# Kernel optimization log

Measured on AMD Instinct MI355X. Metric: run time of the kernel, lower is better.

## Reference

```python
import jax, jax.numpy as jnp
import numpy as np

N, E, B, ROWS, IN, HID, JKO, FEAT, OH, OUT = 200000, 6400000, 64, 128, 128, 6, 4, 2560, 20, 2

def _leaky(x, s):
    return jnp.where(x >= 0, x, s * x)

def _ln(x, g, b, eps=1e-5):
    mu = jnp.mean(x, -1, keepdims=True)
    v = jnp.mean((x - mu) ** 2, -1, keepdims=True)
    return (x - mu) * jax.lax.rsqrt(v + eps) * g + b

def setup_inputs():
    key = jax.random.key(0)
    ks = jax.random.split(key, 32)
    def w(k, shape, fan_in):
        return jax.random.normal(k, shape, jnp.float32) * (1.0 / np.sqrt(fan_in))
    inp = {
        'x': jax.random.normal(ks[0], (N, IN), jnp.float32),
        'edge_index': jax.random.randint(ks[1], (2, E), 0, N, jnp.int32),
        'batch': jnp.sort(jax.random.randint(ks[2], (N,), 0, B, jnp.int32)),
        'features': jax.random.normal(ks[3], (B, ROWS, FEAT), jnp.float32),
        'one_hot': jax.random.uniform(ks[4], (B, OH), jnp.float32),
        # GATv2Conv params (heads=1)
        'W_l': w(ks[5], (IN, HID), IN), 'b_l': jnp.zeros((HID,)),
        'W_r': w(ks[6], (IN, HID), IN), 'b_r': jnp.zeros((HID,)),
        'att': w(ks[7], (HID,), HID), 'conv_b': jnp.zeros((HID,)),
        # BasicGNN final lin after JK (6 -> 4)
        'jk_W': w(ks[8], (HID, JKO), HID), 'jk_b': jnp.zeros((JKO,)),
        # MLP chain on features
        'l1_W': w(ks[9], (FEAT, 256), FEAT), 'l1_b': jnp.zeros((256,)),
        'ln1_g': jnp.ones((256,)), 'ln1_b': jnp.zeros((256,)),
        'l2_W': w(ks[10], (256, 64), 256), 'l2_b': jnp.zeros((64,)),
        'ln2_g': jnp.ones((64,)), 'ln2_b': jnp.zeros((64,)),
        'l3_W': w(ks[11], (64, 8), 64), 'l3_b': jnp.zeros((8,)),
        'ln3_g': jnp.ones((8,)), 'ln3_b': jnp.zeros((8,)),
        # flattening: rows*8 -> 32
        'fl_W': w(ks[12], (ROWS * 8, 32), ROWS * 8), 'fl_b': jnp.zeros((32,)),
        'ln4_g': jnp.ones((32,)), 'ln4_b': jnp.zeros((32,)),
        # output: 4 + 32 + 20 = 56 -> OUT
        'out_W': w(ks[13], (56, OUT), 56), 'out_b': jnp.zeros((OUT,)),
    }
    return inp

def _forward(x, features, one_hot, W_l, b_l, W_r, b_r, att, conv_b, jk_W, jk_b,
             l1_W, l1_b, ln1_g, ln1_b, l2_W, l2_b, ln2_g, ln2_b, l3_W, l3_b, ln3_g, ln3_b,
             fl_W, fl_b, ln4_g, ln4_b, out_W, out_b, edge_index, batch):
    n = x.shape[0]
    # GATv2Conv, heads=1: separate source/target transforms
    xl = x @ W_l + b_l  # [N,6] source/message features
    xr = x @ W_r + b_r  # [N,6] target features
    loops = jnp.arange(n, dtype=edge_index.dtype)
    src = jnp.concatenate([edge_index[0], loops])  # add self loops
    dst = jnp.concatenate([edge_index[1], loops])
    e = _leaky(xl[src] + xr[dst], 0.2)             # [E+N,6]
    score = e @ att                                 # [E+N]
    m = jax.lax.stop_gradient(jax.ops.segment_max(score, dst, num_segments=n))
    p = jnp.exp(score - m[dst])
    z = jax.ops.segment_sum(p, dst, num_segments=n)
    alpha = p / z[dst]                              # segment softmax over incoming edges
    agg = jax.ops.segment_sum(alpha[:, None] * xl[src], dst, num_segments=n) + conv_b
    x1 = _leaky(agg, 0.01)                          # BasicGNN act ('leakyrelu')
    # JK-LSTM with a single layer collapses to identity (softmax over 1 element)
    h = x1 @ jk_W + jk_b                            # [N,4]
    # global mean pool per graph
    nb = features.shape[0]
    sums = jax.ops.segment_sum(h, batch, num_segments=nb)
    cnt = jax.ops.segment_sum(jnp.ones((n,), h.dtype), batch, num_segments=nb)
    xgcn = sums / jnp.maximum(cnt, 1.0)[:, None]    # [B,4]
    # MLP on features (dropout = identity in eval)
    f = _leaky(_ln(features @ l1_W + l1_b, ln1_g, ln1_b), 0.01)
    f = _leaky(_ln(f @ l2_W + l2_b, ln2_g, ln2_b), 0.01)
    f = _leaky(_ln(f @ l3_W + l3_b, ln3_g, ln3_b), 0.01)  # [B,ROWS,8]
    flat = f.reshape(nb, -1)
    xf = _leaky(_ln(flat @ fl_W + fl_b, ln4_g, ln4_b), 0.01)  # [B,32]
    cat = jnp.concatenate([xgcn, xf, one_hot], axis=1)        # [B,56]
    return cat @ out_W + out_b

def reference(x, features, one_hot, W_l, b_l, W_r, b_r, att, conv_b, jk_W, jk_b,
              l1_W, l1_b, ln1_g, ln1_b, l2_W, l2_b, ln2_g, ln2_b, l3_W, l3_b, ln3_g, ln3_b,
              fl_W, fl_b, ln4_g, ln4_b, out_W, out_b, edge_index, batch):
    return _forward(x, features, one_hot, W_l, b_l, W_r, b_r, att, conv_b, jk_W, jk_b,
                    l1_W, l1_b, ln1_g, ln1_b, l2_W, l2_b, ln2_g, ln2_b, l3_W, l3_b, ln3_g, ln3_b,
                    fl_W, fl_b, ln4_g, ln4_b, out_W, out_b, edge_index, batch)
```

## Files before the change

kernel.cpp:

```cpp
#include <hip/hip_runtime.h>
#include <cstdint>
#include <cstddef>

#define N_NODES 200000
#define N_EDGES 6400000
#define NB      64
#define MROWS   8192
#define FEAT    2560

#define BSZ   256
#define NBK   782
#define EBLK  512
#define ETILE 12500
#define BCAP  8960
#define NXB   768
#define GEMMB 256
#define MLPB  64

typedef __attribute__((ext_vector_type(8))) short bf16x8;
typedef __attribute__((ext_vector_type(4))) float f32x4;

__device__ __forceinline__ unsigned short bf16rne(float f) {
    unsigned u = __builtin_bit_cast(unsigned, f);
    u += 0x7fffu + ((u >> 16) & 1u);
    return (unsigned short)(u >> 16);
}

__device__ __forceinline__ float bf16f(unsigned short h) {
    return __builtin_bit_cast(float, (unsigned)h << 16);
}

__device__ __forceinline__ void async_cp16(const void* g, void* l) {
    __builtin_amdgcn_global_load_lds(
        (const __attribute__((address_space(1))) unsigned int*)g,
        (__attribute__((address_space(3))) unsigned int*)l, 16, 0, 0);
}

__device__ __forceinline__ void edge_acc(
    uint4 g, const float* xrd, const float* attv, float& z, float* agg)
{
    float xls[6];
    xls[0] = __builtin_bit_cast(float, g.x << 16);
    xls[1] = __builtin_bit_cast(float, g.x & 0xffff0000u);
    xls[2] = __builtin_bit_cast(float, g.y << 16);
    xls[3] = __builtin_bit_cast(float, g.y & 0xffff0000u);
    xls[4] = __builtin_bit_cast(float, g.z << 16);
    xls[5] = __builtin_bit_cast(float, g.z & 0xffff0000u);
    float sc = 0.f;
#pragma unroll
    for (int j = 0; j < 6; j++) {
        float e = xls[j] + xrd[j];
        e = (e >= 0.f) ? e : 0.2f * e;
        sc += attv[j] * e;
    }
    const float p = __expf(sc);
    z += p;
#pragma unroll
    for (int j = 0; j < 6; j++) agg[j] += p * xls[j];
}


__device__ __forceinline__ void nx_body(
    const int nxi, const int nstride,
    const float* __restrict__ x,
    const float* __restrict__ Wl, const float* __restrict__ bl,
    const float* __restrict__ Wr, const float* __restrict__ br,
    unsigned short* __restrict__ xlb, float* __restrict__ xr)
{
    const int t = threadIdx.x;
    const int l = t & 15;

    float wl[48], wr[48];
#pragma unroll
    for (int q = 0; q < 12; q++) {
        *(float4*)&wl[q * 4] = *(const float4*)(Wl + 48 * l + 4 * q);
        *(float4*)&wr[q * 4] = *(const float4*)(Wr + 48 * l + 4 * q);
    }
    for (int g = nxi; g < N_NODES / 16; g += nstride) {
        const int node = g * 16 + (t >> 4);
        float xv[8];
        *(float4*)&xv[0] = *(const float4*)(x + (size_t)node * 128 + l * 8);
        *(float4*)&xv[4] = *(const float4*)(x + (size_t)node * 128 + l * 8 + 4);

        float al[6] = {}, ar[6] = {};
#pragma unroll
        for (int i = 0; i < 8; i++) {
#pragma unroll
            for (int j = 0; j < 6; j++) {
                al[j] += xv[i] * wl[i * 6 + j];
                ar[j] += xv[i] * wr[i * 6 + j];
            }
        }
#pragma unroll
        for (int off = 8; off >= 1; off >>= 1) {
#pragma unroll
            for (int j = 0; j < 6; j++) {
                al[j] += __shfl_xor(al[j], off);
                ar[j] += __shfl_xor(ar[j], off);
            }
        }
        if (l == 0) {
            union { unsigned short h[8]; uint4 v; } u;
#pragma unroll
            for (int j = 0; j < 6; j++) u.h[j] = bf16rne(al[j] + bl[j]);
            u.h[6] = 0; u.h[7] = 0;
            *(uint4*)(xlb + (size_t)node * 8) = u.v;
            float4 r0; float2 r1;
            r0.x = ar[0] + br[0]; r0.y = ar[1] + br[1];
            r0.z = ar[2] + br[2]; r0.w = ar[3] + br[3];
            r1.x = ar[4] + br[4]; r1.y = ar[5] + br[5];
            *(float4*)(xr + (size_t)node * 8) = r0;
            *(float2*)(xr + (size_t)node * 8 + 4) = r1;
        }
    }
}

__device__ __forceinline__ void eb_body(
    const int bid, char* smem,
    const int* __restrict__ ei, int* __restrict__ cursor, int* __restrict__ pairs)
{
    int* sorted = (int*)smem;
    int* hb     = sorted + ETILE;
    int* cur    = hb + NBK + 1;
    int* gbl    = cur + NBK;
    int* wsum   = gbl + NBK;
    const int t = threadIdx.x;
    const int lane = t & 63, wid = t >> 6;
    const int base = bid * ETILE;

    for (int b = t; b < NBK; b += 256) cur[b] = 0;
    __syncthreads();

    for (int i = t; i < ETILE; i += 256)
        atomicAdd(&cur[ei[N_EDGES + base + i] >> 8], 1);
    __syncthreads();

    int c[4]; int lsum = 0;
#pragma unroll
    for (int q = 0; q < 4; q++) {
        const int b = 4 * t + q;
        c[q] = (b < NBK) ? cur[b] : 0;
        lsum += c[q];
    }
    int v = lsum;
#pragma unroll
    for (int d = 1; d < 64; d <<= 1) {
        const int o = __shfl_up(v, d);
        if (lane >= d) v += o;
    }
    if (lane == 63) wsum[wid] = v;
    __syncthreads();
    int off = 0;
#pragma unroll
    for (int w = 0; w < 3; w++) if (w < wid) off += wsum[w];
    int run = off + v - lsum;

    int mygb[4];
#pragma unroll
    for (int q = 0; q < 4; q++) {
        const int b = 4 * t + q;
        mygb[q] = (b < NBK && c[q] > 0) ? atomicAdd(&cursor[b], c[q]) : 0;
    }

#pragma unroll
    for (int q = 0; q < 4; q++) {
        const int b = 4 * t + q;
        if (b <= NBK) hb[b] = run;
        if (b < NBK) cur[b] = run;
        run += c[q];
    }
    __syncthreads();

    for (int i = t; i < ETILE; i += 256) {
        const int d = ei[N_EDGES + base + i];
        const int s = ei[base + i];
        const int pos = atomicAdd(&cur[d >> 8], 1);
        sorted[pos] = (s << 8) | (d & 255);
    }
#pragma unroll
    for (int q = 0; q < 4; q++) {
        const int b = 4 * t + q;
        if (b < NBK) gbl[b] = mygb[q];
    }
    __syncthreads();

    const int grp = t >> 4, gl = t & 15;
    for (int b = grp; b < NBK; b += 16) {
        const int st = hb[b];
        const int cnt = hb[b + 1] - st;
        int* dst = pairs + b * BCAP + gbl[b];
        for (int i = gl; i < cnt; i += 16)
            dst[i] = sorted[st + i];
    }
}

__device__ __forceinline__ void gemm_l1_body(
    const int bx, const int by, char* smem,
    const float* __restrict__ A, const unsigned short* __restrict__ Bt,
    const float* __restrict__ bias, float* __restrict__ C)
{
    unsigned short (*As)[64 * 64] = (unsigned short(*)[64 * 64])smem;
    unsigned short (*Bs)[128 * 64] =
        (unsigned short(*)[128 * 64])(smem + 2 * 64 * 64 * sizeof(short));
    const int K = FEAT, N = 256;
    const int t = threadIdx.x;
    const int w = t >> 6, l = t & 63;
    const int l15 = l & 15, quad = l >> 4;
    const int wm = (w & 1) * 32, wn = (w >> 1) * 64;
    const int gm0 = bx * 64;
    const int gn0 = by * 128;
    const int r8 = l >> 3;
    const int c8 = (l & 7) ^ r8;
    const int ar = t >> 2;
    const int ac0 = (t & 3) * 2;

    f32x4 acc[2][4];
#pragma unroll
    for (int mt = 0; mt < 2; mt++)
#pragma unroll
        for (int nt = 0; nt < 4; nt++) acc[mt][nt] = (f32x4){0.f, 0.f, 0.f, 0.f};

    const int niter = K / 64;

#pragma unroll
    for (int c = 0; c < 4; c++) {
        const int j = w * 4 + c;
        async_cp16(Bt + (size_t)(gn0 + j * 8 + r8) * K + c8 * 8, &Bs[0][j * 512]);
    }
    {
        const float* src = A + (size_t)(gm0 + ar) * K + ac0 * 8;
        float4 v0 = *(const float4*)src;
        float4 v1 = *(const float4*)(src + 4);
        float4 v2 = *(const float4*)(src + 8);
        float4 v3 = *(const float4*)(src + 12);
        union { unsigned short h[8]; uint4 u; } p0, p1;
        p0.h[0] = bf16rne(v0.x); p0.h[1] = bf16rne(v0.y);
        p0.h[2] = bf16rne(v0.z); p0.h[3] = bf16rne(v0.w);
        p0.h[4] = bf16rne(v1.x); p0.h[5] = bf16rne(v1.y);
        p0.h[6] = bf16rne(v1.z); p0.h[7] = bf16rne(v1.w);
        p1.h[0] = bf16rne(v2.x); p1.h[1] = bf16rne(v2.y);
        p1.h[2] = bf16rne(v2.z); p1.h[3] = bf16rne(v2.w);
        p1.h[4] = bf16rne(v3.x); p1.h[5] = bf16rne(v3.y);
        p1.h[6] = bf16rne(v3.z); p1.h[7] = bf16rne(v3.w);
        *(uint4*)&As[0][ar * 64 + ((ac0 + 0) ^ (ar & 7)) * 8] = p0.u;
        *(uint4*)&As[0][ar * 64 + ((ac0 + 1) ^ (ar & 7)) * 8] = p1.u;
    }

    int p = 0;
    for (int i = 0; i < niter; i++) {
        __syncthreads();
        const bool nxt = (i + 1 < niter);
        float4 v0, v1, v2, v3;
        if (nxt) {
            const int k1 = (i + 1) * 64;
#pragma unroll
            for (int c = 0; c < 4; c++) {
                const int j = w * 4 + c;
                async_cp16(Bt + (size_t)(gn0 + j * 8 + r8) * K + k1 + c8 * 8,
                           &Bs[p ^ 1][j * 512]);
            }
            const float* src = A + (size_t)(gm0 + ar) * K + k1 + ac0 * 8;
            v0 = *(const float4*)src;
            v1 = *(const float4*)(src + 4);
            v2 = *(const float4*)(src + 8);
            v3 = *(const float4*)(src + 12);
        }
#pragma unroll
        for (int kki = 0; kki < 2; kki++) {
            bf16x8 af[2], bfr[4];
#pragma unroll
            for (int mt = 0; mt < 2; mt++) {
                const int m = wm + mt * 16 + l15;
                af[mt] = *(const bf16x8*)&As[p][m * 64 + (((quad + 4 * kki) ^ (m & 7)) * 8)];
            }
#pragma unroll
            for (int nt = 0; nt < 4; nt++) {
                const int n = wn + nt * 16 + l15;
                bfr[nt] = *(const bf16x8*)&Bs[p][n * 64 + (((quad + 4 * kki) ^ (n & 7)) * 8)];
            }
#pragma unroll
            for (int mt = 0; mt < 2; mt++)
#pragma unroll
                for (int nt = 0; nt < 4; nt++)
                    acc[mt][nt] = __builtin_amdgcn_mfma_f32_16x16x32_bf16(
                        af[mt], bfr[nt], acc[mt][nt], 0, 0, 0);
        }
        if (nxt) {
            union { unsigned short h[8]; uint4 u; } p0, p1;
            p0.h[0] = bf16rne(v0.x); p0.h[1] = bf16rne(v0.y);
            p0.h[2] = bf16rne(v0.z); p0.h[3] = bf16rne(v0.w);
            p0.h[4] = bf16rne(v1.x); p0.h[5] = bf16rne(v1.y);
            p0.h[6] = bf16rne(v1.z); p0.h[7] = bf16rne(v1.w);
            p1.h[0] = bf16rne(v2.x); p1.h[1] = bf16rne(v2.y);
            p1.h[2] = bf16rne(v2.z); p1.h[3] = bf16rne(v2.w);
            p1.h[4] = bf16rne(v3.x); p1.h[5] = bf16rne(v3.y);
            p1.h[6] = bf16rne(v3.z); p1.h[7] = bf16rne(v3.w);
            *(uint4*)&As[p ^ 1][ar * 64 + ((ac0 + 0) ^ (ar & 7)) * 8] = p0.u;
            *(uint4*)&As[p ^ 1][ar * 64 + ((ac0 + 1) ^ (ar & 7)) * 8] = p1.u;
        }
        p ^= 1;
    }
#pragma unroll
    for (int nt = 0; nt < 4; nt++) {
        const int col = gn0 + wn + nt * 16 + l15;
        const float bv = bias[col];
#pragma unroll
        for (int mt = 0; mt < 2; mt++)
#pragma unroll
            for (int rr = 0; rr < 4; rr++) {
                const int row = gm0 + wm + mt * 16 + quad * 4 + rr;
                C[(size_t)row * N + col] = acc[mt][nt][rr] + bv;
            }
    }
}

__device__ __forceinline__ void br_body(
    const int bid, char* smem,
    const int* __restrict__ pairs, const int* __restrict__ cursor,
    const unsigned short* __restrict__ xlb, const float* __restrict__ xr,
    const float* __restrict__ att, const float* __restrict__ conv_b,
    const float* __restrict__ jkW, const float* __restrict__ jkb,
    const int* __restrict__ batch,
    float* __restrict__ gsum, float* __restrict__ gcnt)
{
    int* sorted = (int*)smem;
    int* hist   = sorted + BCAP;
    int* wtot   = hist + 256;
    const int t = threadIdx.x;
    const int lane = t & 63, wid = t >> 6;
    const int d0 = bid * BSZ + t;

    float xrd[6];
    if (d0 < N_NODES) {
        float4 a = *(const float4*)(xr + (size_t)d0 * 8);
        float2 b = *(const float2*)(xr + (size_t)d0 * 8 + 4);
        xrd[0] = a.x; xrd[1] = a.y; xrd[2] = a.z;
        xrd[3] = a.w; xrd[4] = b.x; xrd[5] = b.y;
    } else {
#pragma unroll
        for (int j = 0; j < 6; j++) xrd[j] = 0.f;
    }
    float attv[6];
#pragma unroll
    for (int j = 0; j < 6; j++) attv[j] = att[j];

    float z = 0.f, agg[6] = {};
    const uint4* xl4 = (const uint4*)xlb;
    const int e0 = bid * BCAP;
    const int e1 = e0 + cursor[bid];

    for (int c0 = e0; c0 < e1; c0 += BCAP) {
        const int rem = e1 - c0;
        const int cnt_chunk = (rem < BCAP) ? rem : BCAP;
        hist[t] = 0;
        __syncthreads();
        for (int i = t; i < cnt_chunk; i += 256)
            atomicAdd(&hist[pairs[c0 + i] & 255], 1);
        __syncthreads();
        const int h = hist[t];
        int v = h;
#pragma unroll
        for (int d = 1; d < 64; d <<= 1) {
            int o = __shfl_up(v, d);
            if (lane >= d) v += o;
        }
        if (lane == 63) wtot[wid] = v;
        __syncthreads();
        int off = 0;
#pragma unroll
        for (int wv = 0; wv < 3; wv++) if (wv < wid) off += wtot[wv];
        const int my_start = v - h + off;
        const int my_cnt = h;
        __syncthreads();
        hist[t] = my_start;
        __syncthreads();
        for (int i = t; i < cnt_chunk; i += 256) {
            const int pv = pairs[c0 + i];
            const int pos = atomicAdd(&hist[pv & 255], 1);
            sorted[pos] = ((unsigned)pv) >> 8;
        }
        __syncthreads();
        int i = 0;
        for (; i + 4 <= my_cnt; i += 4) {
            const int s0 = sorted[my_start + i];
            const int s1 = sorted[my_start + i + 1];
            const int s2 = sorted[my_start + i + 2];
            const int s3 = sorted[my_start + i + 3];
            const uint4 g0 = xl4[s0], g1 = xl4[s1], g2 = xl4[s2], g3 = xl4[s3];
            edge_acc(g0, xrd, attv, z, agg);
            edge_acc(g1, xrd, attv, z, agg);
            edge_acc(g2, xrd, attv, z, agg);
            edge_acc(g3, xrd, attv, z, agg);
        }
        for (; i < my_cnt; i++) {
            const uint4 g = xl4[sorted[my_start + i]];
            edge_acc(g, xrd, attv, z, agg);
        }
        __syncthreads();
    }

    float hh[4] = {0.f, 0.f, 0.f, 0.f};
    float cw = 0.f;
    int b = 0;
    if (d0 < N_NODES) {
        const uint4 g = xl4[d0];
        float xld[6];
        xld[0] = __builtin_bit_cast(float, g.x << 16);
        xld[1] = __builtin_bit_cast(float, g.x & 0xffff0000u);
        xld[2] = __builtin_bit_cast(float, g.y << 16);
        xld[3] = __builtin_bit_cast(float, g.y & 0xffff0000u);
        xld[4] = __builtin_bit_cast(float, g.z << 16);
        xld[5] = __builtin_bit_cast(float, g.z & 0xffff0000u);
        float sc = 0.f;
#pragma unroll
        for (int j = 0; j < 6; j++) {
            float e = xld[j] + xrd[j];
            e = (e >= 0.f) ? e : 0.2f * e;
            sc += attv[j] * e;
        }
        const float p = __expf(sc);
        const float zz = z + p;
#pragma unroll
        for (int c = 0; c < 4; c++) hh[c] = jkb[c];
#pragma unroll
        for (int j = 0; j < 6; j++) {
            float aj = (agg[j] + p * xld[j]) / zz + conv_b[j];
            aj = (aj >= 0.f) ? aj : 0.01f * aj;
#pragma unroll
            for (int c = 0; c < 4; c++) hh[c] += aj * jkW[j * 4 + c];
        }
        b = batch[d0];
        cw = 1.f;
    }
    const int b0 = __shfl(b, 0);
    if (__all(b == b0)) {
#pragma unroll
        for (int off2 = 32; off2 >= 1; off2 >>= 1) {
#pragma unroll
            for (int c = 0; c < 4; c++) hh[c] += __shfl_xor(hh[c], off2);
            cw += __shfl_xor(cw, off2);
        }
        if (lane == 0 && cw > 0.f) {
#pragma unroll
            for (int c = 0; c < 4; c++) atomicAdd(gsum + b0 * 4 + c, hh[c]);
            atomicAdd(gcnt + b0, cw);
        }
    } else if (cw > 0.f) {
#pragma unroll
        for (int c = 0; c < 4; c++) atomicAdd(gsum + b * 4 + c, hh[c]);
        atomicAdd(gcnt + b, cw);
    }
}

__device__ __forceinline__ void mlp_body(
    const int g, char* smem,
    const float* __restrict__ f1, const unsigned short* __restrict__ w2t,
    const float* __restrict__ ln1_g, const float* __restrict__ ln1_b,
    const float* __restrict__ l2_b,
    const float* __restrict__ ln2_g, const float* __restrict__ ln2_b,
    const float* __restrict__ l3_W, const float* __restrict__ l3_b,
    const float* __restrict__ ln3_g, const float* __restrict__ ln3_b,
    const float* __restrict__ fl_W, const float* __restrict__ fl_b,
    const float* __restrict__ ln4_g, const float* __restrict__ ln4_b,
    float* __restrict__ xf)
{
    unsigned short* W2 = (unsigned short*)smem;
    float* f3s = (float*)(smem + 32768);
    float* sp  = (float*)(smem + 32768 + 4096);
    const int t = threadIdx.x;
    const int w = t >> 6, l = t & 63;

    for (int i = t; i < 16384; i += 256) {
        const int j = i >> 8, k = i & 255;
        W2[k * 64 + j] = w2t[i];
    }
    const float4 g1 = *(const float4*)(ln1_g + 4 * l);
    const float4 b1 = *(const float4*)(ln1_b + 4 * l);
    const float bo2 = l2_b[l], g2 = ln2_g[l], b2 = ln2_b[l];
    float w3r[8];
    *(float4*)&w3r[0] = *(const float4*)(l3_W + l * 8);
    *(float4*)&w3r[4] = *(const float4*)(l3_W + l * 8 + 4);
    float g3[8], b3[8], bo3[8];
#pragma unroll
    for (int c = 0; c < 8; c++) {
        g3[c] = ln3_g[c]; b3[c] = ln3_b[c]; bo3[c] = l3_b[c];
    }
    __syncthreads();

    for (int r = w; r < 128; r += 4) {
        const size_t row = (size_t)g * 128 + r;
        const float4 v = *(const float4*)(f1 + row * 256 + 4 * l);
        float s = v.x + v.y + v.z + v.w;
        float s2 = v.x * v.x + v.y * v.y + v.z * v.z + v.w * v.w;
#pragma unroll
        for (int o = 32; o >= 1; o >>= 1) {
            s += __shfl_xor(s, o);
            s2 += __shfl_xor(s2, o);
        }
        const float mu = s * (1.0f / 256.0f);
        const float rs = rsqrtf(s2 * (1.0f / 256.0f) - mu * mu + 1e-5f);
        float y[4];
        y[0] = (v.x - mu) * rs * g1.x + b1.x;
        y[1] = (v.y - mu) * rs * g1.y + b1.y;
        y[2] = (v.z - mu) * rs * g1.z + b1.z;
        y[3] = (v.w - mu) * rs * g1.w + b1.w;
#pragma unroll
        for (int i = 0; i < 4; i++) y[i] = (y[i] >= 0.f) ? y[i] : 0.01f * y[i];

        float acc = bo2;
#pragma unroll 4
        for (int k0 = 0; k0 < 64; k0++) {
            const float yv0 = __shfl(y[0], k0);
            const float yv1 = __shfl(y[1], k0);
            const float yv2 = __shfl(y[2], k0);
            const float yv3 = __shfl(y[3], k0);
            const int kb = k0 * 256 + l;
            acc += yv0 * bf16f(W2[kb]);
            acc += yv1 * bf16f(W2[kb + 64]);
            acc += yv2 * bf16f(W2[kb + 128]);
            acc += yv3 * bf16f(W2[kb + 192]);
        }
        float s1 = acc, q1 = acc * acc;
#pragma unroll
        for (int o = 32; o >= 1; o >>= 1) {
            s1 += __shfl_xor(s1, o);
            q1 += __shfl_xor(q1, o);
        }
        const float mu2 = s1 * (1.0f / 64.0f);
        const float rs2 = rsqrtf(q1 * (1.0f / 64.0f) - mu2 * mu2 + 1e-5f);
        float y2 = (acc - mu2) * rs2 * g2 + b2;
        y2 = (y2 >= 0.f) ? y2 : 0.01f * y2;

        float p8[8];
#pragma unroll
        for (int c = 0; c < 8; c++) p8[c] = y2 * w3r[c];
#pragma unroll
        for (int o = 32; o >= 1; o >>= 1)
#pragma unroll
            for (int c = 0; c < 8; c++) p8[c] += __shfl_xor(p8[c], o);
#pragma unroll
        for (int c = 0; c < 8; c++) p8[c] += bo3[c];
        float s3 = 0.f;
#pragma unroll
        for (int c = 0; c < 8; c++) s3 += p8[c];
        const float mu3 = s3 * 0.125f;
        float q3 = 0.f;
#pragma unroll
        for (int c = 0; c < 8; c++) { const float d = p8[c] - mu3; q3 += d * d; }
        const float rs3 = rsqrtf(q3 * 0.125f + 1e-5f);
        if (l == 0) {
            float o8[8];
#pragma unroll
            for (int c = 0; c < 8; c++) {
                float yy = (p8[c] - mu3) * rs3 * g3[c] + b3[c];
                o8[c] = (yy >= 0.f) ? yy : 0.01f * yy;
            }
            *(float4*)&f3s[r * 8] = *(float4*)&o8[0];
            *(float4*)&f3s[r * 8 + 4] = *(float4*)&o8[4];
        }
    }
    __syncthreads();

    const int c = t & 31, part = t >> 5;
    float facc = 0.f;
    for (int k = part * 128; k < part * 128 + 128; k++)
        facc += f3s[k] * fl_W[k * 32 + c];
    sp[part * 32 + c] = facc;
    __syncthreads();
    if (t < 32) {
        float vv = fl_b[t];
#pragma unroll
        for (int p = 0; p < 8; p++) vv += sp[p * 32 + t];
        float ss = vv, ss2 = vv * vv;
#pragma unroll
        for (int o = 16; o >= 1; o >>= 1) {
            ss += __shfl_xor(ss, o);
            ss2 += __shfl_xor(ss2, o);
        }
        const float mu4 = ss * (1.0f / 32.0f);
        const float var4 = ss2 * (1.0f / 32.0f) - mu4 * mu4;
        float yy = (vv - mu4) * rsqrtf(var4 + 1e-5f) * ln4_g[t] + ln4_b[t];
        xf[g * 32 + t] = (yy >= 0.f) ? yy : 0.01f * yy;
    }
}


__global__ __launch_bounds__(256) void node_xform(
    const float* __restrict__ x,
    const float* __restrict__ Wl, const float* __restrict__ bl,
    const float* __restrict__ Wr, const float* __restrict__ br,
    unsigned short* __restrict__ xlb, float* __restrict__ xr)
{
    nx_body(blockIdx.x, N_NODES / 16, x, Wl, bl, Wr, br, xlb, xr);
}

__global__ __launch_bounds__(256) void edge_bucket(
    const int* __restrict__ ei, int* __restrict__ cursor, int* __restrict__ pairs)
{
    __shared__ __align__(16) char smem[59408];
    eb_body(blockIdx.x, smem, ei, cursor, pairs);
}

__global__ __launch_bounds__(256) void mfma_gemm_l1(
    const float* __restrict__ A, const unsigned short* __restrict__ Bt,
    const float* __restrict__ bias, float* __restrict__ C)
{
    __shared__ __align__(16) char smem[49152];
    gemm_l1_body(blockIdx.x, blockIdx.y, smem, A, Bt, bias, C);
}

__global__ __launch_bounds__(256) void bucket_reduce(
    const int* __restrict__ pairs, const int* __restrict__ cursor,
    const unsigned short* __restrict__ xlb, const float* __restrict__ xr,
    const float* __restrict__ att, const float* __restrict__ conv_b,
    const float* __restrict__ jkW, const float* __restrict__ jkb,
    const int* __restrict__ batch,
    float* __restrict__ gsum, float* __restrict__ gcnt)
{
    __shared__ __align__(16) char smem[36880];
    br_body(blockIdx.x, smem, pairs, cursor, xlb, xr, att, conv_b, jkW, jkb,
            batch, gsum, gcnt);
}

__global__ __launch_bounds__(256) void fused_front(
    const float* __restrict__ x,
    const float* __restrict__ Wl, const float* __restrict__ bl,
    const float* __restrict__ Wr, const float* __restrict__ br,
    unsigned short* __restrict__ xlb, float* __restrict__ xr,
    const int* __restrict__ ei, int* __restrict__ cursor, int* __restrict__ pairs,
    const float* __restrict__ A, const unsigned short* __restrict__ Bt,
    const float* __restrict__ bias, float* __restrict__ C)
{
    __shared__ __align__(16) char smem[59408];
    const int bid = blockIdx.x;
    const int role = bid % 3;
    const int q = bid / 3;
    if (role == 0) {
        eb_body(q, smem, ei, cursor, pairs);
    } else if (role == 1 && q < GEMMB) {
        gemm_l1_body(q & 127, q >> 7, smem, A, Bt, bias, C);
    } else {
        const int nxi = (role == 2) ? q : EBLK + (q - GEMMB);
        nx_body(nxi, NXB, x, Wl, bl, Wr, br, xlb, xr);
    }
}

__global__ __launch_bounds__(256, 4) void fused_back(
    const int* __restrict__ pairs, const int* __restrict__ cursor,
    const unsigned short* __restrict__ xlb, const float* __restrict__ xr,
    const float* __restrict__ att, const float* __restrict__ conv_b,
    const float* __restrict__ jkW, const float* __restrict__ jkb,
    const int* __restrict__ batch,
    float* __restrict__ gsum, float* __restrict__ gcnt,
    const float* __restrict__ f1, const unsigned short* __restrict__ w2t,
    const float* __restrict__ ln1_g, const float* __restrict__ ln1_b,
    const float* __restrict__ l2_b,
    const float* __restrict__ ln2_g, const float* __restrict__ ln2_b,
    const float* __restrict__ l3_W, const float* __restrict__ l3_b,
    const float* __restrict__ ln3_g, const float* __restrict__ ln3_b,
    const float* __restrict__ fl_W, const float* __restrict__ fl_b,
    const float* __restrict__ ln4_g, const float* __restrict__ ln4_b,
    float* __restrict__ xf)
{
    __shared__ __align__(16) char smem[37888];
    const int bid = blockIdx.x;
    const int q = bid / 13, r = bid % 13;
    if (r == 0 && q < MLPB) {
        mlp_body(q, smem, f1, w2t, ln1_g, ln1_b, l2_b, ln2_g, ln2_b,
                 l3_W, l3_b, ln3_g, ln3_b, fl_W, fl_b, ln4_g, ln4_b, xf);
    } else {
        const int brid = bid - ((q < MLPB) ? (q + (r > 0 ? 1 : 0)) : MLPB);
        br_body(brid, smem, pairs, cursor, xlb, xr, att, conv_b, jkW, jkb,
                batch, gsum, gcnt);
    }
}

__global__ __launch_bounds__(256) void castT(
    const float* __restrict__ W, unsigned short* __restrict__ Wt, int K, int N)
{
    const int k = blockIdx.x * 256 + threadIdx.x;
    const int n = blockIdx.y;
    if (k < K) Wt[(size_t)n * K + k] = bf16rne(W[(size_t)k * N + n]);
}


__global__ __launch_bounds__(256) void mfma_gemm_l2(
    const unsigned short* __restrict__ Ab, const unsigned short* __restrict__ Bt,
    const float* __restrict__ bias, float* __restrict__ C,
    int M, int N, int K)
{
    __shared__ unsigned short As[32 * 64];
    __shared__ unsigned short Bs[64 * 64];
    const int t = threadIdx.x;
    const int w = t >> 6, l = t & 63;
    const int l15 = l & 15, quad = l >> 4;
    const int gm0 = blockIdx.x * 32;
    const int gn0 = blockIdx.y * 64;
    const int r8 = l >> 3;
    const int c8 = (l & 7) ^ r8;

    f32x4 acc[2];
    acc[0] = (f32x4){0.f, 0.f, 0.f, 0.f};
    acc[1] = (f32x4){0.f, 0.f, 0.f, 0.f};

    for (int k0 = 0; k0 < K; k0 += 64) {
#pragma unroll
        for (int c = 0; c < 2; c++) {
            const int j = w * 2 + c;
            async_cp16(Bt + (size_t)(gn0 + j * 8 + r8) * K + k0 + c8 * 8,
                       &Bs[j * 512]);
        }
        async_cp16(Ab + (size_t)(gm0 + w * 8 + r8) * K + k0 + c8 * 8, &As[w * 512]);
        __syncthreads();
#pragma unroll
        for (int kki = 0; kki < 2; kki++) {
            bf16x8 af[2], bfr;
#pragma unroll
            for (int mt = 0; mt < 2; mt++) {
                const int m = mt * 16 + l15;
                af[mt] = *(const bf16x8*)&As[m * 64 + (((quad + 4 * kki) ^ (m & 7)) * 8)];
            }
            const int n = w * 16 + l15;
            bfr = *(const bf16x8*)&Bs[n * 64 + (((quad + 4 * kki) ^ (n & 7)) * 8)];
#pragma unroll
            for (int mt = 0; mt < 2; mt++)
                acc[mt] = __builtin_amdgcn_mfma_f32_16x16x32_bf16(
                    af[mt], bfr, acc[mt], 0, 0, 0);
        }
        __syncthreads();
    }
    const int col = gn0 + w * 16 + l15;
    const float bv = bias[col];
#pragma unroll
    for (int mt = 0; mt < 2; mt++)
#pragma unroll
        for (int rr = 0; rr < 4; rr++) {
            const int row = gm0 + mt * 16 + quad * 4 + rr;
            C[(size_t)row * N + col] = acc[mt][rr] + bv;
        }
}

__global__ __launch_bounds__(256) void ln_leaky_c256(
    const float* __restrict__ f, unsigned short* __restrict__ out,
    const float* __restrict__ g, const float* __restrict__ b)
{
    const int row = blockIdx.x;
    const int t = threadIdx.x;
    float v = f[(size_t)row * 256 + t];
    float s = v, s2 = v * v;
#pragma unroll
    for (int off = 32; off >= 1; off >>= 1) {
        s += __shfl_xor(s, off);
        s2 += __shfl_xor(s2, off);
    }
    __shared__ float ws[4], ws2[4];
    const int wid = t >> 6, lane = t & 63;
    if (lane == 0) { ws[wid] = s; ws2[wid] = s2; }
    __syncthreads();
    const float S = ws[0] + ws[1] + ws[2] + ws[3];
    const float S2 = ws2[0] + ws2[1] + ws2[2] + ws2[3];
    const float mu = S * (1.0f / 256.0f);
    const float var = S2 * (1.0f / 256.0f) - mu * mu;
    float y = (v - mu) * rsqrtf(var + 1e-5f) * g[t] + b[t];
    y = (y >= 0.f) ? y : 0.01f * y;
    out[(size_t)row * 256 + t] = bf16rne(y);
}

__global__ __launch_bounds__(256) void ln_leaky_c64(
    float* __restrict__ f, const float* __restrict__ g, const float* __restrict__ b)
{
    const int wid = threadIdx.x >> 6, lane = threadIdx.x & 63;
    const int row = blockIdx.x * 4 + wid;
    float v = f[(size_t)row * 64 + lane];
    float s = v, s2 = v * v;
#pragma unroll
    for (int off = 32; off >= 1; off >>= 1) {
        s += __shfl_xor(s, off);
        s2 += __shfl_xor(s2, off);
    }
    const float mu = s * (1.0f / 64.0f);
    const float var = s2 * (1.0f / 64.0f) - mu * mu;
    float y = (v - mu) * rsqrtf(var + 1e-5f) * g[lane] + b[lane];
    f[(size_t)row * 64 + lane] = (y >= 0.f) ? y : 0.01f * y;
}

__global__ __launch_bounds__(256) void l3_ln_leaky(
    const float* __restrict__ f2, const float* __restrict__ W3,
    const float* __restrict__ b3,
    const float* __restrict__ g, const float* __restrict__ b,
    float* __restrict__ f3)
{
    __shared__ float sW[64 * 8];
    const int t = threadIdx.x;
    sW[t] = W3[t]; sW[t + 256] = W3[t + 256];
    __syncthreads();
    const int row = blockIdx.x * 32 + (t >> 3);
    const int c = t & 7;
    float acc = b3[c];
    const float* fr = f2 + (size_t)row * 64;
#pragma unroll 8
    for (int k = 0; k < 64; k++) acc += fr[k] * sW[k * 8 + c];
    float s = acc, s2 = acc * acc;
#pragma unroll
    for (int off = 4; off >= 1; off >>= 1) {
        s += __shfl_xor(s, off);
        s2 += __shfl_xor(s2, off);
    }
    const float mu = s * (1.0f / 8.0f);
    const float var = s2 * (1.0f / 8.0f) - mu * mu;
    float y = (acc - mu) * rsqrtf(var + 1e-5f) * g[c] + b[c];
    f3[(size_t)row * 8 + c] = (y >= 0.f) ? y : 0.01f * y;
}

__global__ __launch_bounds__(256) void flat_ln_leaky(
    const float* __restrict__ f3, const float* __restrict__ W,
    const float* __restrict__ bb,
    const float* __restrict__ g, const float* __restrict__ b,
    float* __restrict__ xf)
{
    __shared__ float sf[1024];
    __shared__ float sp[8][32];
    const int t = threadIdx.x;
    const int gb = blockIdx.x;
    *(float4*)&sf[t * 4] = *(const float4*)(f3 + (size_t)gb * 1024 + t * 4);
    __syncthreads();
    const int c = t & 31, part = t >> 5;
    float acc = 0.f;
    for (int k = part * 128; k < part * 128 + 128; k++) acc += sf[k] * W[k * 32 + c];
    sp[part][c] = acc;
    __syncthreads();
    if (t < 32) {
        float v = bb[t];
#pragma unroll
        for (int p = 0; p < 8; p++) v += sp[p][t];
        float s = v, s2 = v * v;
#pragma unroll
        for (int off = 16; off >= 1; off >>= 1) {
            s += __shfl_xor(s, off);
            s2 += __shfl_xor(s2, off);
        }
        const float mu = s * (1.0f / 32.0f);
        const float var = s2 * (1.0f / 32.0f) - mu * mu;
        float y = (v - mu) * rsqrtf(var + 1e-5f) * g[t] + b[t];
        xf[gb * 32 + t] = (y >= 0.f) ? y : 0.01f * y;
    }
}

__global__ __launch_bounds__(128) void final_out(
    const float* __restrict__ gsum, const float* __restrict__ gcnt,
    const float* __restrict__ xf, const float* __restrict__ onehot,
    const float* __restrict__ Wo, const float* __restrict__ bo,
    float* __restrict__ out)
{
    const int t = threadIdx.x;
    const int gb = t >> 1, o = t & 1;
    float cnt = gcnt[gb];
    cnt = (cnt > 1.f) ? cnt : 1.f;
    float acc = bo[o];
#pragma unroll
    for (int j = 0; j < 4; j++)  acc += (gsum[gb * 4 + j] / cnt) * Wo[j * 2 + o];
#pragma unroll
    for (int j = 0; j < 32; j++) acc += xf[gb * 32 + j] * Wo[(4 + j) * 2 + o];
#pragma unroll
    for (int j = 0; j < 20; j++) acc += onehot[gb * 20 + j] * Wo[(36 + j) * 2 + o];
    out[t] = acc;
}

extern "C" void kernel_launch(void* const* d_in, const int* in_sizes, int n_in,
                              void* d_out, int out_size, void* d_ws, size_t ws_size,
                              hipStream_t stream)
{
    const float* x        = (const float*)d_in[0];
    const int*   ei       = (const int*)d_in[1];
    const int*   batch    = (const int*)d_in[2];
    const float* features = (const float*)d_in[3];
    const float* one_hot  = (const float*)d_in[4];
    const float* W_l   = (const float*)d_in[5];
    const float* b_l   = (const float*)d_in[6];
    const float* W_r   = (const float*)d_in[7];
    const float* b_r   = (const float*)d_in[8];
    const float* att   = (const float*)d_in[9];
    const float* conv_b = (const float*)d_in[10];
    const float* jk_W  = (const float*)d_in[11];
    const float* jk_b  = (const float*)d_in[12];
    const float* l1_W  = (const float*)d_in[13];
    const float* l1_b  = (const float*)d_in[14];
    const float* ln1_g = (const float*)d_in[15];
    const float* ln1_b = (const float*)d_in[16];
    const float* l2_W  = (const float*)d_in[17];
    const float* l2_b  = (const float*)d_in[18];
    const float* ln2_g = (const float*)d_in[19];
    const float* ln2_b = (const float*)d_in[20];
    const float* l3_W  = (const float*)d_in[21];
    const float* l3_b  = (const float*)d_in[22];
    const float* ln3_g = (const float*)d_in[23];
    const float* ln3_b = (const float*)d_in[24];
    const float* fl_W  = (const float*)d_in[25];
    const float* fl_b  = (const float*)d_in[26];
    const float* ln4_g = (const float*)d_in[27];
    const float* ln4_b = (const float*)d_in[28];
    const float* out_W = (const float*)d_in[29];
    const float* out_b = (const float*)d_in[30];
    (void)in_sizes; (void)n_in; (void)out_size;

    float* ws = (float*)d_ws;
    unsigned short* xlb = (unsigned short*)(ws + 0);
    float* xr   = ws + 800000;
    unsigned short* w1t = (unsigned short*)(ws + 2400000);
    unsigned short* w2t = (unsigned short*)(ws + 2727680);
    float* gsum   = ws + 2735872;
    float* gcnt   = ws + 2736128;
    int*   cursor = (int*)(ws + 2736192);
    int* pairs = (int*)(ws + 2737024);

    const bool fuse = ws_size >= (size_t)13481344 * 4;

    hipMemsetAsync(gsum, 0, 1102 * sizeof(float), stream);

    castT<<<dim3(10, 256), 256, 0, stream>>>(l1_W, w1t, FEAT, 256);
    castT<<<dim3(1, 64), 256, 0, stream>>>(l2_W, w2t, 256, 64);

    if (fuse) {
        float* f1 = ws + 9743744;
        float* xf = ws + 13479296;
        fused_front<<<EBLK + GEMMB + NXB, 256, 0, stream>>>(
            x, W_l, b_l, W_r, b_r, xlb, xr,
            ei, cursor, pairs,
            features, w1t, l1_b, f1);
        fused_back<<<NBK + MLPB, 256, 0, stream>>>(
            pairs, cursor, xlb, xr, att, conv_b, jk_W, jk_b, batch,
            gsum, gcnt,
            f1, w2t, ln1_g, ln1_b, l2_b, ln2_g, ln2_b,
            l3_W, l3_b, ln3_g, ln3_b, fl_W, fl_b, ln4_g, ln4_b, xf);
        final_out<<<1, 128, 0, stream>>>(gsum, gcnt, xf, one_hot, out_W, out_b,
                                         (float*)d_out);
    } else {
        float* f1           = ws + 2737024;
        unsigned short* f1b = (unsigned short*)(ws + 4834176);
        float* f2           = ws + 5358464;
        float* f3           = ws + 5882752;
        float* xf           = ws + 5948288;
        node_xform<<<N_NODES / 16, 256, 0, stream>>>(x, W_l, b_l, W_r, b_r,
                                                     xlb, xr);
        edge_bucket<<<EBLK, 256, 0, stream>>>(ei, cursor, pairs);
        bucket_reduce<<<NBK, 256, 0, stream>>>(pairs, cursor, xlb, xr, att,
                                               conv_b, jk_W, jk_b, batch,
                                               gsum, gcnt);
        mfma_gemm_l1<<<dim3(MROWS / 64, 2), 256, 0, stream>>>(
            features, w1t, l1_b, f1);
        ln_leaky_c256<<<MROWS, 256, 0, stream>>>(f1, f1b, ln1_g, ln1_b);
        mfma_gemm_l2<<<dim3(MROWS / 32, 1), 256, 0, stream>>>(
            f1b, w2t, l2_b, f2, MROWS, 64, 256);
        ln_leaky_c64<<<MROWS / 4, 256, 0, stream>>>(f2, ln2_g, ln2_b);
        l3_ln_leaky<<<MROWS / 32, 256, 0, stream>>>(f2, l3_W, l3_b,
                                                    ln3_g, ln3_b, f3);
        flat_ln_leaky<<<NB, 256, 0, stream>>>(f3, fl_W, fl_b, ln4_g, ln4_b, xf);
        final_out<<<1, 128, 0, stream>>>(gsum, gcnt, xf, one_hot, out_W, out_b,
                                         (float*)d_out);
    }
}
```

Baseline: 651.7 us.

## Split MLP tail into many row blocks and move flatten into final kernel

Measured after the change: 561.3 us. -13.9%, faster.

```diff
diff --git a/kernel.cpp b/kernel.cpp
--- a/kernel.cpp
+++ b/kernel.cpp
@@ -15,7 +15,7 @@
 #define BCAP  8960
 #define NXB   768
 #define GEMMB 256
-#define MLPB  64
+#define MLPRB 512
 
 typedef __attribute__((ext_vector_type(8))) short bf16x8;
 typedef __attribute__((ext_vector_type(4))) float f32x4;
@@ -452,27 +452,23 @@
     }
 }
 
-__device__ __forceinline__ void mlp_body(
-    const int g, char* smem,
+__device__ __forceinline__ void mlp_rows_body(
+    const int bid, char* smem,
     const float* __restrict__ f1, const unsigned short* __restrict__ w2t,
     const float* __restrict__ ln1_g, const float* __restrict__ ln1_b,
     const float* __restrict__ l2_b,
     const float* __restrict__ ln2_g, const float* __restrict__ ln2_b,
     const float* __restrict__ l3_W, const float* __restrict__ l3_b,
     const float* __restrict__ ln3_g, const float* __restrict__ ln3_b,
-    const float* __restrict__ fl_W, const float* __restrict__ fl_b,
-    const float* __restrict__ ln4_g, const float* __restrict__ ln4_b,
-    float* __restrict__ xf)
+    float* __restrict__ f3)
 {
     unsigned short* W2 = (unsigned short*)smem;
-    float* f3s = (float*)(smem + 32768);
-    float* sp  = (float*)(smem + 32768 + 4096);
     const int t = threadIdx.x;
     const int w = t >> 6, l = t & 63;
 
     for (int i = t; i < 16384; i += 256) {
         const int j = i >> 8, k = i & 255;
-        W2[k * 64 + j] = w2t[i];
+        W2[k * 66 + j] = w2t[i];
     }
     const float4 g1 = *(const float4*)(ln1_g + 4 * l);
     const float4 b1 = *(const float4*)(ln1_b + 4 * l);
@@ -487,9 +483,10 @@
     }
     __syncthreads();
 
-    for (int r = w; r < 128; r += 4) {
-        const size_t row = (size_t)g * 128 + r;
-        const float4 v = *(const float4*)(f1 + row * 256 + 4 * l);
+#pragma unroll 1
+    for (int i4 = 0; i4 < 4; i4++) {
+        const int row = bid * 16 + w * 4 + i4;
+        const float4 v = *(const float4*)(f1 + (size_t)row * 256 + 4 * l);
         float s = v.x + v.y + v.z + v.w;
         float s2 = v.x * v.x + v.y * v.y + v.z * v.z + v.w * v.w;
 #pragma unroll
@@ -514,11 +511,11 @@
             const float yv1 = __shfl(y[1], k0);
             const float yv2 = __shfl(y[2], k0);
             const float yv3 = __shfl(y[3], k0);
-            const int kb = k0 * 256 + l;
+            const int kb = k0 * 264 + l;
             acc += yv0 * bf16f(W2[kb]);
-            acc += yv1 * bf16f(W2[kb + 64]);
-            acc += yv2 * bf16f(W2[kb + 128]);
-            acc += yv3 * bf16f(W2[kb + 192]);
+            acc += yv1 * bf16f(W2[kb + 66]);
+            acc += yv2 * bf16f(W2[kb + 132]);
+            acc += yv3 * bf16f(W2[kb + 198]);
         }
         float s1 = acc, q1 = acc * acc;
 #pragma unroll
@@ -555,32 +552,9 @@
                 float yy = (p8[c] - mu3) * rs3 * g3[c] + b3[c];
                 o8[c] = (yy >= 0.f) ? yy : 0.01f * yy;
             }
-            *(float4*)&f3s[r * 8] = *(float4*)&o8[0];
-            *(float4*)&f3s[r * 8 + 4] = *(float4*)&o8[4];
-        }
-    }
-    __syncthreads();
-
-    const int c = t & 31, part = t >> 5;
-    float facc = 0.f;
-    for (int k = part * 128; k < part * 128 + 128; k++)
-        facc += f3s[k] * fl_W[k * 32 + c];
-    sp[part * 32 + c] = facc;
-    __syncthreads();
-    if (t < 32) {
-        float vv = fl_b[t];
-#pragma unroll
-        for (int p = 0; p < 8; p++) vv += sp[p * 32 + t];
-        float ss = vv, ss2 = vv * vv;
-#pragma unroll
-        for (int o = 16; o >= 1; o >>= 1) {
-            ss += __shfl_xor(ss, o);
-            ss2 += __shfl_xor(ss2, o);
-        }
-        const float mu4 = ss * (1.0f / 32.0f);
-        const float var4 = ss2 * (1.0f / 32.0f) - mu4 * mu4;
-        float yy = (vv - mu4) * rsqrtf(var4 + 1e-5f) * ln4_g[t] + ln4_b[t];
-        xf[g * 32 + t] = (yy >= 0.f) ? yy : 0.01f * yy;
+            *(float4*)(f3 + (size_t)row * 8) = *(float4*)&o8[0];
+            *(float4*)(f3 + (size_t)row * 8 + 4) = *(float4*)&o8[4];
+        }
     }
 }
 
@@ -658,20 +632,68 @@
     const float* __restrict__ ln2_g, const float* __restrict__ ln2_b,
     const float* __restrict__ l3_W, const float* __restrict__ l3_b,
     const float* __restrict__ ln3_g, const float* __restrict__ ln3_b,
-    const float* __restrict__ fl_W, const float* __restrict__ fl_b,
-    const float* __restrict__ ln4_g, const float* __restrict__ ln4_b,
-    float* __restrict__ xf)
-{
-    __shared__ __align__(16) char smem[37888];
+    float* __restrict__ f3)
+{
+    __shared__ __align__(16) char smem[36880];
     const int bid = blockIdx.x;
-    const int q = bid / 13, r = bid % 13;
-    if (r == 0 && q < MLPB) {
-        mlp_body(q, smem, f1, w2t, ln1_g, ln1_b, l2_b, ln2_g, ln2_b,
-                 l3_W, l3_b, ln3_g, ln3_b, fl_W, fl_b, ln4_g, ln4_b, xf);
+    if (bid < NBK) {
+        br_body(bid, smem, pairs, cursor, xlb, xr, att, conv_b, jkW, jkb,
+                batch, gsum, gcnt);
     } else {
-        const int brid = bid - ((q < MLPB) ? (q + (r > 0 ? 1 : 0)) : MLPB);
-        br_body(brid, smem, pairs, cursor, xlb, xr, att, conv_b, jkW, jkb,
-                batch, gsum, gcnt);
+        mlp_rows_body(bid - NBK, smem, f1, w2t, ln1_g, ln1_b, l2_b,
+                      ln2_g, ln2_b, l3_W, l3_b, ln3_g, ln3_b, f3);
+    }
+}
+
+__global__ __launch_bounds__(256) void flat_final(
+    const float* __restrict__ f3, const float* __restrict__ W,
+    const float* __restrict__ bb,
+    const float* __restrict__ g, const float* __restrict__ b,
+    const float* __restrict__ gsum, const float* __restrict__ gcnt,
+    const float* __restrict__ onehot,
+    const float* __restrict__ Wo, const float* __restrict__ bo,
+    float* __restrict__ out)
+{
+    __shared__ float sf[1024];
+    __shared__ float sp[8][32];
+    __shared__ float sxf[32];
+    const int t = threadIdx.x;
+    const int gb = blockIdx.x;
+    *(float4*)&sf[t * 4] = *(const float4*)(f3 + (size_t)gb * 1024 + t * 4);
+    __syncthreads();
+    const int c = t & 31, part = t >> 5;
+    float acc = 0.f;
+    for (int k = part * 128; k < part * 128 + 128; k++) acc += sf[k] * W[k * 32 + c];
+    sp[part][c] = acc;
+    __syncthreads();
+    if (t < 32) {
+        float v = bb[t];
+#pragma unroll
+        for (int p = 0; p < 8; p++) v += sp[p][t];
+        float s = v, s2 = v * v;
+#pragma unroll
+        for (int off = 16; off >= 1; off >>= 1) {
+            s += __shfl_xor(s, off);
+            s2 += __shfl_xor(s2, off);
+        }
+        const float mu = s * (1.0f / 32.0f);
+        const float var = s2 * (1.0f / 32.0f) - mu * mu;
+        float y = (v - mu) * rsqrtf(var + 1e-5f) * g[t] + b[t];
+        sxf[t] = (y >= 0.f) ? y : 0.01f * y;
+    }
+    __syncthreads();
+    if (t < 2) {
+        const int o = t;
+        float cnt = gcnt[gb];
+        cnt = (cnt > 1.f) ? cnt : 1.f;
+        float a2 = bo[o];
+#pragma unroll
+        for (int j = 0; j < 4; j++)  a2 += (gsum[gb * 4 + j] / cnt) * Wo[j * 2 + o];
+#pragma unroll
+        for (int j = 0; j < 32; j++) a2 += sxf[j] * Wo[(4 + j) * 2 + o];
+#pragma unroll
+        for (int j = 0; j < 20; j++) a2 += onehot[gb * 20 + j] * Wo[(36 + j) * 2 + o];
+        out[gb * 2 + o] = a2;
     }
 }
 
@@ -922,18 +944,19 @@
 
     if (fuse) {
         float* f1 = ws + 9743744;
-        float* xf = ws + 13479296;
+        float* f3 = ws + 13413760;
         fused_front<<<EBLK + GEMMB + NXB, 256, 0, stream>>>(
             x, W_l, b_l, W_r, b_r, xlb, xr,
             ei, cursor, pairs,
             features, w1t, l1_b, f1);
-        fused_back<<<NBK + MLPB, 256, 0, stream>>>(
+        fused_back<<<NBK + MLPRB, 256, 0, stream>>>(
             pairs, cursor, xlb, xr, att, conv_b, jk_W, jk_b, batch,
             gsum, gcnt,
             f1, w2t, ln1_g, ln1_b, l2_b, ln2_g, ln2_b,
-            l3_W, l3_b, ln3_g, ln3_b, fl_W, fl_b, ln4_g, ln4_b, xf);
-        final_out<<<1, 128, 0, stream>>>(gsum, gcnt, xf, one_hot, out_W, out_b,
-                                         (float*)d_out);
+            l3_W, l3_b, ln3_g, ln3_b, f3);
+        flat_final<<<NB, 256, 0, stream>>>(
+            f3, fl_W, fl_b, ln4_g, ln4_b,
+            gsum, gcnt, one_hot, out_W, out_b, (float*)d_out);
     } else {
         float* f1           = ws + 2737024;
         unsigned short* f1b = (unsigned short*)(ws + 4834176);
```
